# Kernel optimization log

Hardware: AMD Instinct MI355X
Metric: run time of the kernel (lower is better)

The kernel has to match this reference:

```python
import jax, jax.numpy as jnp
import numpy as np

EPS = 1e-12  # F.normalize eps

def _l2norm(x, axis=-1):
    n = jnp.sqrt(jnp.sum(x * x, axis=axis, keepdims=True))
    return x / jnp.maximum(n, EPS)

def setup_inputs() -> dict:
    key = jax.random.key(0)
    k1, k2 = jax.random.split(key)
    N, D, C = 262144, 128, 1024
    embeddings = jax.random.normal(k1, (N, D), dtype=jnp.float32)
    labels = jax.random.randint(k2, (N,), 0, C, dtype=jnp.int64)
    return {"embeddings": embeddings, "labels": labels, "num_classes": C}

def reference(embeddings, labels, num_classes):
    # Normalize all embeddings: [N, D]
    emb = _l2norm(embeddings, axis=1)
    # Per-class segment sums and counts (replaces python loop over unique labels)
    sums = jax.ops.segment_sum(emb, labels, num_segments=num_classes)          # [C, D]
    counts = jax.ops.segment_sum(jnp.ones((emb.shape[0],), emb.dtype), labels,
                                 num_segments=num_classes)                     # [C]
    safe_counts = jnp.maximum(counts, 1.0)
    prototypes = _l2norm(sums / safe_counts[:, None], axis=1)                  # [C, D]
    # cosine sim of each sample to its class prototype
    sim = jnp.sum(emb * prototypes[labels], axis=1)                           # [N]
    # per-class mean of (1 - sim)
    loss_sums = jax.ops.segment_sum(1.0 - sim, labels, num_segments=num_classes)
    per_class = loss_sums / safe_counts                                        # [C]
    valid = (counts >= 2.0).astype(emb.dtype)                                  # classes with >=2 samples
    n_valid = jnp.sum(valid)
    loss = jnp.sum(per_class * valid) / jnp.maximum(n_valid, 1.0)
    return jnp.where(n_valid > 0, loss, jnp.zeros((), emb.dtype))
```

## Files before the change

kernel.cpp:

```cpp
#include <hip/hip_runtime.h>
#include <math.h>

#define NUM_CLASSES 1024

__device__ __forceinline__ int get_label(const int* __restrict__ l, int i, int mode32) {
    return l[mode32 ? i : (i << 1)] & (NUM_CLASSES - 1);
}

__global__ void detect_kernel(const int* __restrict__ labels32,
                              int* __restrict__ flag) {
    int i = threadIdx.x;
    if (labels32[2 * i + 1] != 0) atomicOr(flag, 1);
}

__global__ void hist_kernel(const int* __restrict__ labels, int n,
                            int* __restrict__ counts,
                            const int* __restrict__ flag) {
    __shared__ int h[NUM_CLASSES];
    const int mode32 = *flag;
    for (int i = threadIdx.x; i < NUM_CLASSES; i += blockDim.x) h[i] = 0;
    __syncthreads();
    for (int i = blockIdx.x * blockDim.x + threadIdx.x; i < n;
         i += gridDim.x * blockDim.x) {
        atomicAdd(&h[get_label(labels, i, mode32)], 1);
    }
    __syncthreads();
    for (int i = threadIdx.x; i < NUM_CLASSES; i += blockDim.x) {
        int v = h[i];
        if (v) atomicAdd(&counts[i], v);
    }
}

__global__ void scan_kernel(const int* __restrict__ counts,
                            int* __restrict__ offsets,
                            int* __restrict__ cursor) {
    __shared__ int tmp[NUM_CLASSES];
    int tid = threadIdx.x;
    int v = counts[tid];
    tmp[tid] = v;
    __syncthreads();
    for (int off = 1; off < NUM_CLASSES; off <<= 1) {
        int add = (tid >= off) ? tmp[tid - off] : 0;
        __syncthreads();
        tmp[tid] += add;
        __syncthreads();
    }
    int excl = tmp[tid] - v;
    offsets[tid] = excl;
    cursor[tid]  = excl;
}

__global__ void scatter_kernel(const int* __restrict__ labels, int n,
                               int* __restrict__ cursor,
                               int* __restrict__ sorted,
                               const int* __restrict__ flag) {
    const int mode32 = *flag;
    int i = blockIdx.x * blockDim.x + threadIdx.x;
    if (i < n) {
        int pos = atomicAdd(&cursor[get_label(labels, i, mode32)], 1);
        sorted[pos] = i;
    }
}

#define WPB 8
__global__ __launch_bounds__(512) void class_sum_kernel(
        const float* __restrict__ emb,
        const int* __restrict__ sorted,
        const int* __restrict__ offsets,
        const int* __restrict__ counts,
        float* __restrict__ accum) {
    const int c     = blockIdx.x;
    const int start = offsets[c];
    const int count = counts[c];
    const int wave  = threadIdx.x >> 6;
    const int lane  = threadIdx.x & 63;

    float a0 = 0.0f, a1 = 0.0f;
    for (int r = wave; r < count; r += WPB) {
        const int idx = sorted[start + r];
        const float2 v = *(const float2*)(emb + (size_t)idx * 128 + 2 * lane);
        float sq = v.x * v.x + v.y * v.y;
        #pragma unroll
        for (int off = 32; off; off >>= 1) sq += __shfl_xor(sq, off, 64);
        float inv = 1.0f / fmaxf(sqrtf(sq), 1e-12f);
        a0 += v.x * inv;
        a1 += v.y * inv;
    }

    __shared__ float2 s2[WPB][64];
    s2[wave][lane] = make_float2(a0, a1);
    __syncthreads();

    __shared__ float red[128];
    if (threadIdx.x < 128) {
        int l = threadIdx.x >> 1;
        int hi = threadIdx.x & 1;
        float t = 0.0f;
        #pragma unroll
        for (int w = 0; w < WPB; w++) {
            float2 v = s2[w][l];
            t += hi ? v.y : v.x;
        }
        red[threadIdx.x] = t * t;
    }
    __syncthreads();
    if (threadIdx.x < 64) {
        float x = red[threadIdx.x] + red[threadIdx.x + 64];
        #pragma unroll
        for (int off = 32; off; off >>= 1) x += __shfl_xor(x, off, 64);
        if (threadIdx.x == 0 && count >= 2) {
            float nrm = sqrtf(x);
            float per_class = ((float)count - nrm) / (float)count;
            atomicAdd(&accum[0], per_class);
            atomicAdd(&accum[1], 1.0f);
        }
    }
}

__global__ void finalize_kernel(const float* __restrict__ accum,
                                float* __restrict__ out) {
    if (threadIdx.x == 0 && blockIdx.x == 0) {
        float nv = accum[1];
        out[0] = (nv > 0.0f) ? (accum[0] / nv) : 0.0f;
    }
}

extern "C" void kernel_launch(void* const* d_in, const int* in_sizes, int n_in,
                              void* d_out, int out_size, void* d_ws, size_t ws_size,
                              hipStream_t stream) {
    const float* emb  = (const float*)d_in[0];
    const int* labels = (const int*)d_in[1];

    const int n = in_sizes[1];

    char* ws = (char*)d_ws;
    int*   counts  = (int*)(ws + 0);
    int*   offsets = (int*)(ws + 4096);
    int*   cursor  = (int*)(ws + 8192);
    float* accum   = (float*)(ws + 12288);
    int*   flag    = (int*)(ws + 12304);
    int*   sorted  = (int*)(ws + 16384);

    hipMemsetAsync(ws, 0, 4096, stream);
    hipMemsetAsync(ws + 12288, 0, 32, stream);

    detect_kernel<<<1, 128, 0, stream>>>(labels, flag);
    hist_kernel<<<256, 256, 0, stream>>>(labels, n, counts, flag);
    scan_kernel<<<1, NUM_CLASSES, 0, stream>>>(counts, offsets, cursor);
    scatter_kernel<<<(n + 255) / 256, 256, 0, stream>>>(labels, n, cursor, sorted, flag);
    class_sum_kernel<<<NUM_CLASSES, 512, 0, stream>>>(emb, sorted, offsets, counts, accum);
    finalize_kernel<<<1, 64, 0, stream>>>(accum, (float*)d_out);
}
```

Measured before the change: 295.9 us.

## Use per-block histograms for local-atomic scatter and float4 row loads

The counting sort now writes a histogram per chunk, and the scan kernel turns those into per-block starting offsets. Scatter can then use shared-memory atomics in place of contended global atomics on 1024 cursors. Separately, class_sum now has 16 lanes per row with float4 loads, so each wave handles four rows at a time and needs fewer shuffle steps. The risk is the serial per-class loop over 128 partials in the single-block scan, plus extra workspace traffic for the partials.

After: 261.7 us. 1.13x faster.

```diff
diff --git a/kernel.cpp b/kernel.cpp
--- a/kernel.cpp
+++ b/kernel.cpp
@@ -2,6 +2,7 @@
 #include <math.h>
 
 #define NUM_CLASSES 1024
+#define HIST_CHUNK 2048
 
 __device__ __forceinline__ int get_label(const int* __restrict__ l, int i, int mode32) {
     return l[mode32 ? i : (i << 1)] & (NUM_CLASSES - 1);
@@ -14,51 +15,64 @@
 }
 
 __global__ void hist_kernel(const int* __restrict__ labels, int n,
-                            int* __restrict__ counts,
+                            int* __restrict__ partials,
                             const int* __restrict__ flag) {
     __shared__ int h[NUM_CLASSES];
     const int mode32 = *flag;
     for (int i = threadIdx.x; i < NUM_CLASSES; i += blockDim.x) h[i] = 0;
     __syncthreads();
-    for (int i = blockIdx.x * blockDim.x + threadIdx.x; i < n;
-         i += gridDim.x * blockDim.x) {
-        atomicAdd(&h[get_label(labels, i, mode32)], 1);
+    const int base = blockIdx.x * HIST_CHUNK;
+    for (int k = threadIdx.x; k < HIST_CHUNK; k += blockDim.x) {
+        int i = base + k;
+        if (i < n) atomicAdd(&h[get_label(labels, i, mode32)], 1);
     }
     __syncthreads();
-    for (int i = threadIdx.x; i < NUM_CLASSES; i += blockDim.x) {
-        int v = h[i];
-        if (v) atomicAdd(&counts[i], v);
+    for (int c = threadIdx.x; c < NUM_CLASSES; c += blockDim.x)
+        partials[blockIdx.x * NUM_CLASSES + c] = h[c];
+}
+
+__global__ void scan_kernel(int* __restrict__ partials, int numBlocks,
+                            int* __restrict__ offsets,
+                            int* __restrict__ counts) {
+    __shared__ int tmp[NUM_CLASSES];
+    const int c = threadIdx.x;
+    int sum = 0;
+    for (int b = 0; b < numBlocks; b++) sum += partials[b * NUM_CLASSES + c];
+    tmp[c] = sum;
+    __syncthreads();
+    for (int off = 1; off < NUM_CLASSES; off <<= 1) {
+        int add = (c >= off) ? tmp[c - off] : 0;
+        __syncthreads();
+        tmp[c] += add;
+        __syncthreads();
+    }
+    const int excl = tmp[c] - sum;
+    offsets[c] = excl;
+    counts[c]  = sum;
+    int running = excl;
+    for (int b = 0; b < numBlocks; b++) {
+        int p = partials[b * NUM_CLASSES + c];
+        partials[b * NUM_CLASSES + c] = running;
+        running += p;
     }
 }
 
-__global__ void scan_kernel(const int* __restrict__ counts,
-                            int* __restrict__ offsets,
-                            int* __restrict__ cursor) {
-    __shared__ int tmp[NUM_CLASSES];
-    int tid = threadIdx.x;
-    int v = counts[tid];
-    tmp[tid] = v;
-    __syncthreads();
-    for (int off = 1; off < NUM_CLASSES; off <<= 1) {
-        int add = (tid >= off) ? tmp[tid - off] : 0;
-        __syncthreads();
-        tmp[tid] += add;
-        __syncthreads();
-    }
-    int excl = tmp[tid] - v;
-    offsets[tid] = excl;
-    cursor[tid]  = excl;
-}
-
 __global__ void scatter_kernel(const int* __restrict__ labels, int n,
-                               int* __restrict__ cursor,
+                               const int* __restrict__ partials,
                                int* __restrict__ sorted,
                                const int* __restrict__ flag) {
+    __shared__ int cur[NUM_CLASSES];
     const int mode32 = *flag;
-    int i = blockIdx.x * blockDim.x + threadIdx.x;
-    if (i < n) {
-        int pos = atomicAdd(&cursor[get_label(labels, i, mode32)], 1);
-        sorted[pos] = i;
+    for (int c = threadIdx.x; c < NUM_CLASSES; c += blockDim.x)
+        cur[c] = partials[blockIdx.x * NUM_CLASSES + c];
+    __syncthreads();
+    const int base = blockIdx.x * HIST_CHUNK;
+    for (int k = threadIdx.x; k < HIST_CHUNK; k += blockDim.x) {
+        int i = base + k;
+        if (i < n) {
+            int pos = atomicAdd(&cur[get_label(labels, i, mode32)], 1);
+            sorted[pos] = i;
+        }
     }
 }
 
@@ -74,34 +88,46 @@
     const int count = counts[c];
     const int wave  = threadIdx.x >> 6;
     const int lane  = threadIdx.x & 63;
+    const int g     = lane >> 4;
+    const int sub   = lane & 15;
 
-    float a0 = 0.0f, a1 = 0.0f;
-    for (int r = wave; r < count; r += WPB) {
+    float4 aLo = make_float4(0.f, 0.f, 0.f, 0.f);
+    float4 aHi = make_float4(0.f, 0.f, 0.f, 0.f);
+
+    for (int r = wave * 4 + g; r < count; r += WPB * 4) {
         const int idx = sorted[start + r];
-        const float2 v = *(const float2*)(emb + (size_t)idx * 128 + 2 * lane);
-        float sq = v.x * v.x + v.y * v.y;
-        #pragma unroll
-        for (int off = 32; off; off >>= 1) sq += __shfl_xor(sq, off, 64);
+        const float4* row = (const float4*)(emb + (size_t)idx * 128);
+        float4 v0 = row[sub];
+        float4 v1 = row[sub + 16];
+        float sq = v0.x*v0.x + v0.y*v0.y + v0.z*v0.z + v0.w*v0.w
+                 + v1.x*v1.x + v1.y*v1.y + v1.z*v1.z + v1.w*v1.w;
+        sq += __shfl_xor(sq, 1, 64);
+        sq += __shfl_xor(sq, 2, 64);
+        sq += __shfl_xor(sq, 4, 64);
+        sq += __shfl_xor(sq, 8, 64);
         float inv = 1.0f / fmaxf(sqrtf(sq), 1e-12f);
-        a0 += v.x * inv;
-        a1 += v.y * inv;
+        aLo.x += v0.x * inv; aLo.y += v0.y * inv; aLo.z += v0.z * inv; aLo.w += v0.w * inv;
+        aHi.x += v1.x * inv; aHi.y += v1.y * inv; aHi.z += v1.z * inv; aHi.w += v1.w * inv;
     }
 
-    __shared__ float2 s2[WPB][64];
-    s2[wave][lane] = make_float2(a0, a1);
+    __shared__ float s[WPB * 4][16][8];
+    {
+        float* dst = s[wave * 4 + g][sub];
+        dst[0] = aLo.x; dst[1] = aLo.y; dst[2] = aLo.z; dst[3] = aLo.w;
+        dst[4] = aHi.x; dst[5] = aHi.y; dst[6] = aHi.z; dst[7] = aHi.w;
+    }
     __syncthreads();
 
     __shared__ float red[128];
     if (threadIdx.x < 128) {
-        int l = threadIdx.x >> 1;
-        int hi = threadIdx.x & 1;
+        const int d  = threadIdx.x;
+        const int dd = d & 63;
+        const int sb = dd >> 2;
+        const int j  = (d >> 6) * 4 + (dd & 3);
         float t = 0.0f;
         #pragma unroll
-        for (int w = 0; w < WPB; w++) {
-            float2 v = s2[w][l];
-            t += hi ? v.y : v.x;
-        }
-        red[threadIdx.x] = t * t;
+        for (int k = 0; k < WPB * 4; k++) t += s[k][sb][j];
+        red[d] = t * t;
     }
     __syncthreads();
     if (threadIdx.x < 64) {
@@ -130,24 +156,23 @@
                               hipStream_t stream) {
     const float* emb  = (const float*)d_in[0];
     const int* labels = (const int*)d_in[1];
-
     const int n = in_sizes[1];
+    const int numBlocks = (n + HIST_CHUNK - 1) / HIST_CHUNK;
 
     char* ws = (char*)d_ws;
-    int*   counts  = (int*)(ws + 0);
-    int*   offsets = (int*)(ws + 4096);
-    int*   cursor  = (int*)(ws + 8192);
-    float* accum   = (float*)(ws + 12288);
-    int*   flag    = (int*)(ws + 12304);
-    int*   sorted  = (int*)(ws + 16384);
+    int*   counts   = (int*)(ws + 0);
+    int*   offsets  = (int*)(ws + 4096);
+    float* accum    = (float*)(ws + 8192);
+    int*   flag     = (int*)(ws + 8208);
+    int*   sorted   = (int*)(ws + 16384);
+    int*   partials = (int*)(ws + 16384 + (size_t)n * 4);
 
-    hipMemsetAsync(ws, 0, 4096, stream);
-    hipMemsetAsync(ws + 12288, 0, 32, stream);
+    hipMemsetAsync(ws + 8192, 0, 32, stream);
 
     detect_kernel<<<1, 128, 0, stream>>>(labels, flag);
-    hist_kernel<<<256, 256, 0, stream>>>(labels, n, counts, flag);
-    scan_kernel<<<1, NUM_CLASSES, 0, stream>>>(counts, offsets, cursor);
-    scatter_kernel<<<(n + 255) / 256, 256, 0, stream>>>(labels, n, cursor, sorted, flag);
+    hist_kernel<<<numBlocks, 256, 0, stream>>>(labels, n, partials, flag);
+    scan_kernel<<<1, NUM_CLASSES, 0, stream>>>(partials, numBlocks, offsets, counts);
+    scatter_kernel<<<numBlocks, 256, 0, stream>>>(labels, n, partials, sorted, flag);
     class_sum_kernel<<<NUM_CLASSES, 512, 0, stream>>>(emb, sorted, offsets, counts, accum);
     finalize_kernel<<<1, 64, 0, stream>>>(accum, (float*)d_out);
 }
```
